# Optimization experiments

Measured on AMD Instinct MI355X. Metric: run time of the kernel, lower is better.

Reference implementation:

```python
import jax, jax.numpy as jnp
import numpy as np

B, S, DIM = 2, 2048, 2048
H, DK, DR, DC, DCP, DV = 16, 128, 64, 512, 1024, 128


def setup_inputs() -> dict:
    key = jax.random.key(0)
    ks = jax.random.split(key, 8)
    s = 0.02  # weight init scale
    return {
        "x": jax.random.normal(ks[0], (B, S, DIM), jnp.float32),
        "W_c": jax.random.normal(ks[1], (DIM, DC), jnp.float32) * s,
        "W_c_prime": jax.random.normal(ks[2], (DIM, DCP), jnp.float32) * s,
        "W_qc": jax.random.normal(ks[3], (H, DCP, DK), jnp.float32) * s,
        "W_qr": jax.random.normal(ks[4], (H, DCP, DR), jnp.float32) * s,
        "W_kc": jax.random.normal(ks[5], (H, DC, DK), jnp.float32) * s,
        "W_kr": jax.random.normal(ks[6], (DIM, DR), jnp.float32) * s,
        "W_v": jax.random.normal(ks[7], (H, DC, DV), jnp.float32) * s,
    }


def reference(x, W_c, W_c_prime, W_qc, W_qr, W_kc, W_kr, W_v):
    # Latent compressions
    c = x @ W_c                 # [B,S,DC]  compressed KV latent
    cp = x @ W_c_prime          # [B,S,DCP] compressed Q latent
    # Per-head projections, vectorized over heads
    q_c = jnp.einsum('bsc,hck->bhsk', cp, W_qc)   # [B,H,S,DK]
    q_r = jnp.einsum('bsc,hcr->bhsr', cp, W_qr)   # [B,H,S,DR]
    k_c = jnp.einsum('bsc,hck->bhsk', c, W_kc)    # [B,H,S,DK]
    k_r = x @ W_kr                                 # [B,S,DR] shared across heads
    q = jnp.concatenate([q_c, q_r], axis=-1)                               # [B,H,S,DK+DR]
    k = jnp.concatenate([k_c, jnp.broadcast_to(k_r[:, None], (B, H, S, DR))], axis=-1)
    scale = 1.0 / np.sqrt(DK + DR)
    scores = jnp.einsum('bhsd,bhtd->bhst', q, k) * scale                   # [B,H,S,S]
    causal = jnp.tril(jnp.ones((S, S), dtype=bool))
    scores = jnp.where(causal, scores, -jnp.inf)
    probs = jax.nn.softmax(scores.astype(jnp.float32), axis=-1).astype(q.dtype)
    v = jnp.einsum('bsc,hcv->bhsv', c, W_v)                                # [B,H,S,DV]
    out = jnp.einsum('bhst,bhtv->bhsv', probs, v)                          # [B,H,S,DV]
    return out.transpose(0, 2, 1, 3).reshape(B, S, H * DV)                 # concat heads
```

## Files before the change

### kernel.cpp

```cpp
#include <hip/hip_runtime.h>
#include <stdint.h>

typedef __bf16 bf16;
typedef __bf16 bfx8 __attribute__((ext_vector_type(8)));
typedef __bf16 bfx4 __attribute__((ext_vector_type(4)));
typedef float floatx4 __attribute__((ext_vector_type(4)));

#define B_ 2
#define S_ 2048
#define DIM_ 2048
#define H_ 16
#define DK_ 128
#define DR_ 64
#define DC_ 512
#define DCP_ 1024
#define DV_ 128
#define DQK_ 192

#define MASK_VAL (-30000.0f)
#define C1_ 0.10411754f

__global__ void k_prep(
    const float* __restrict__ x, bf16* __restrict__ xb,
    const float* __restrict__ W_c, const float* __restrict__ W_cp,
    const float* __restrict__ W_qc, const float* __restrict__ W_qr,
    const float* __restrict__ W_kc, const float* __restrict__ W_kr,
    const float* __restrict__ W_v,
    bf16* __restrict__ Wt_c, bf16* __restrict__ Wt_cp,
    bf16* __restrict__ Wt_qc, bf16* __restrict__ Wt_qr,
    bf16* __restrict__ Wt_kc, bf16* __restrict__ Wt_kr,
    bf16* __restrict__ Wt_v) {
    __shared__ float tile[32][33];
    int bid0 = blockIdx.x;
    if (bid0 < 4096) {
        size_t i = ((size_t)bid0 * 256 + threadIdx.x) * 8;
        float4 a = *(const float4*)(x + i);
        float4 b = *(const float4*)(x + i + 4);
        bfx8 r;
        r[0] = (bf16)a.x; r[1] = (bf16)a.y; r[2] = (bf16)a.z; r[3] = (bf16)a.w;
        r[4] = (bf16)b.x; r[5] = (bf16)b.y; r[6] = (bf16)b.z; r[7] = (bf16)b.w;
        *(bfx8*)(xb + i) = r;
        return;
    }
    int bid = bid0 - 4096;
    const float* in; bf16* out; int K, N, lx, ly, local;
    if (bid < 1024)      { in = W_c;  out = Wt_c;  K = 2048; N = 512;  lx = 4; ly = 6; local = bid; }
    else if (bid < 3072) { in = W_cp; out = Wt_cp; K = 2048; N = 1024; lx = 5; ly = 6; local = bid - 1024; }
    else if (bid < 5120) { in = W_qc; out = Wt_qc; K = 1024; N = 128;  lx = 2; ly = 5; local = bid - 3072; }
    else if (bid < 6144) { in = W_qr; out = Wt_qr; K = 1024; N = 64;   lx = 1; ly = 5; local = bid - 5120; }
    else if (bid < 7168) { in = W_kc; out = Wt_kc; K = 512;  N = 128;  lx = 2; ly = 4; local = bid - 6144; }
    else if (bid < 7296) { in = W_kr; out = Wt_kr; K = 2048; N = 64;   lx = 1; ly = 6; local = bid - 7168; }
    else                 { in = W_v;  out = Wt_v;  K = 512;  N = 128;  lx = 2; ly = 4; local = bid - 7296; }
    int n0 = (local & ((1 << lx) - 1)) << 5;
    int k0 = ((local >> lx) & ((1 << ly) - 1)) << 5;
    int h  = local >> (lx + ly);
    const float* ip = in + (size_t)h * K * N;
    bf16* op = out + (size_t)h * K * N;
    int tx = threadIdx.x & 31, ty = threadIdx.x >> 5;
#pragma unroll
    for (int i = 0; i < 32; i += 8)
        tile[ty + i][tx] = ip[(size_t)(k0 + ty + i) * N + (n0 + tx)];
    __syncthreads();
#pragma unroll
    for (int i = 0; i < 32; i += 8)
        op[(size_t)(n0 + ty + i) * K + (k0 + tx)] = (bf16)tile[tx][ty + i];
}

__device__ __forceinline__ void gld16(const bf16* g, bf16* l) {
    __builtin_amdgcn_global_load_lds(
        (const __attribute__((address_space(1))) void*)g,
        (__attribute__((address_space(3))) void*)l, 16, 0, 0);
}

__device__ __forceinline__ bfx8 frag_ld(const bf16* lds, int row, int quad) {
    int pb = quad ^ ((row >> 1) & 3);
    return *(const bfx8*)(lds + row * 32 + pb * 8);
}

#define SLICE_ 4096

__device__ __forceinline__ void gemm_core(const bf16* __restrict__ A,
                                          const bf16* __restrict__ Bt,
                                          int K, int rowlimB,
                                          floatx4 acc[4][4],
                                          bf16* A_lds, bf16* B_lds) {
    int tid = threadIdx.x, wave = tid >> 6, lane = tid & 63;
    int l15 = lane & 15, quad = lane >> 4;
    int wm = (wave & 1) * 64, wn = (wave >> 1) * 64;
    int ch0 = wave * 2, ch1 = wave * 2 + 1;
    int r0 = ch0 * 16 + (lane >> 2), r1 = ch1 * 16 + (lane >> 2);
    int kb0 = (lane & 3) ^ ((r0 >> 1) & 3), kb1 = (lane & 3) ^ ((r1 >> 1) & 3);
    int rb0 = r0 <= rowlimB ? r0 : rowlimB;
    int rb1 = r1 <= rowlimB ? r1 : rowlimB;
    const bf16* a0 = A + (size_t)r0 * K + kb0 * 8;
    const bf16* a1 = A + (size_t)r1 * K + kb1 * 8;
    const bf16* b0 = Bt + (size_t)rb0 * K + kb0 * 8;
    const bf16* b1 = Bt + (size_t)rb1 * K + kb1 * 8;
    bf16* da0 = A_lds + ch0 * 512;
    bf16* da1 = A_lds + ch1 * 512;
    bf16* db0 = B_lds + ch0 * 512;
    bf16* db1 = B_lds + ch1 * 512;
    for (int k0 = 0; k0 < K; k0 += 64) {
        __syncthreads();
        gld16(a0 + k0, da0);
        gld16(a1 + k0, da1);
        gld16(b0 + k0, db0);
        gld16(b1 + k0, db1);
        gld16(a0 + k0 + 32, da0 + SLICE_);
        gld16(a1 + k0 + 32, da1 + SLICE_);
        gld16(b0 + k0 + 32, db0 + SLICE_);
        gld16(b1 + k0 + 32, db1 + SLICE_);
        __syncthreads();
#pragma unroll
        for (int sl = 0; sl < 2; ++sl) {
            const bf16* As = A_lds + sl * SLICE_;
            const bf16* Bs = B_lds + sl * SLICE_;
            bfx8 a[4], b[4];
#pragma unroll
            for (int t = 0; t < 4; ++t) a[t] = frag_ld(As, wm + t * 16 + l15, quad);
#pragma unroll
            for (int t = 0; t < 4; ++t) b[t] = frag_ld(Bs, wn + t * 16 + l15, quad);
#pragma unroll
            for (int mt = 0; mt < 4; ++mt)
#pragma unroll
                for (int nt = 0; nt < 4; ++nt)
                    acc[mt][nt] = __builtin_amdgcn_mfma_f32_16x16x32_bf16(
                        a[mt], b[nt], acc[mt][nt], 0, 0, 0);
        }
    }
}

__global__ __launch_bounds__(256, 3) void k_gemm1(
    const bf16* __restrict__ xb, const bf16* __restrict__ Wt_c,
    const bf16* __restrict__ Wt_cp, const bf16* __restrict__ Wt_kr,
    bf16* __restrict__ c_ws, bf16* __restrict__ cp_ws, bf16* __restrict__ kr_ws) {
    __shared__ __attribute__((aligned(16))) bf16 A_lds[2 * SLICE_];
    __shared__ __attribute__((aligned(16))) bf16 B_lds[2 * SLICE_];
    int hw = blockIdx.x + 13 * blockIdx.y;
    int virt = (hw & 7) * 52 + (hw >> 3);
    int bx = virt % 13, by = virt / 13;
    const bf16* Bt; bf16* outp; int ldc, col0, rowlim;
    if (bx < 4)       { Bt = Wt_c  + (size_t)bx * 128 * DIM_;       outp = c_ws;  ldc = DC_;  col0 = bx * 128;       rowlim = 127; }
    else if (bx < 12) { Bt = Wt_cp + (size_t)(bx - 4) * 128 * DIM_; outp = cp_ws; ldc = DCP_; col0 = (bx - 4) * 128; rowlim = 127; }
    else              { Bt = Wt_kr;                                  outp = kr_ws; ldc = DR_;  col0 = 0;              rowlim = 63;  }
    floatx4 acc[4][4];
#pragma unroll
    for (int i = 0; i < 4; ++i)
#pragma unroll
        for (int j = 0; j < 4; ++j) acc[i][j] = (floatx4){0.f, 0.f, 0.f, 0.f};
    gemm_core(xb + (size_t)by * 128 * DIM_, Bt, DIM_, rowlim, acc, A_lds, B_lds);
    int tid = threadIdx.x, wave = tid >> 6, lane = tid & 63;
    int l15 = lane & 15, quad = lane >> 4;
    int wm = (wave & 1) * 64, wn = (wave >> 1) * 64;
#pragma unroll
    for (int mt = 0; mt < 4; ++mt)
#pragma unroll
        for (int nt = 0; nt < 4; ++nt) {
            int n = wn + nt * 16 + l15;
            if (n > rowlim) continue;
#pragma unroll
            for (int r = 0; r < 4; ++r) {
                int m = by * 128 + wm + mt * 16 + quad * 4 + r;
                outp[(size_t)m * ldc + col0 + n] = (bf16)acc[mt][nt][r];
            }
        }
}

__global__ __launch_bounds__(256, 3) void k_gemm23(
    const bf16* __restrict__ cp_ws, const bf16* __restrict__ c_ws,
    const bf16* __restrict__ Wt_qc, const bf16* __restrict__ Wt_qr,
    const bf16* __restrict__ Wt_kc, const bf16* __restrict__ Wt_v,
    bf16* __restrict__ q_ws, bf16* __restrict__ kc_ws, bf16* __restrict__ vt_ws) {
    __shared__ __attribute__((aligned(16))) bf16 A_lds[2 * SLICE_];
    __shared__ __attribute__((aligned(16))) bf16 B_lds[2 * SLICE_];
    int hw = blockIdx.x;
    int virt = (hw & 7) * 224 + (hw >> 3);
    int tid = threadIdx.x, wave = tid >> 6, lane = tid & 63;
    int l15 = lane & 15, quad = lane >> 4;
    int wm = (wave & 1) * 64, wn = (wave >> 1) * 64;
    floatx4 acc[4][4];
#pragma unroll
    for (int i = 0; i < 4; ++i)
#pragma unroll
        for (int j = 0; j < 4; ++j) acc[i][j] = (floatx4){0.f, 0.f, 0.f, 0.f};
    if (virt < 768) {
        int bx = virt % 3, by = (virt / 3) & 31, hz = virt / 96;
        const bf16* Bt;
        if (bx < 2) Bt = Wt_qc + (size_t)(hz * 2 + bx) * DK_ * DCP_;
        else        Bt = Wt_qr + (size_t)hz * 128 * DCP_;
        gemm_core(cp_ws + (size_t)by * 128 * DCP_, Bt, DCP_, 127, acc, A_lds, B_lds);
#pragma unroll
        for (int mt = 0; mt < 4; ++mt)
#pragma unroll
            for (int nt = 0; nt < 4; ++nt) {
                int n = wn + nt * 16 + l15;
                int h, col;
                if (bx < 2) { h = hz * 2 + bx;        col = n; }
                else        { h = hz * 2 + (n >> 6);  col = 128 + (n & 63); }
#pragma unroll
                for (int r = 0; r < 4; ++r) {
                    int m = by * 128 + wm + mt * 16 + quad * 4 + r;
                    int b = m >> 11, s = m & 2047;
                    q_ws[(((size_t)b * H_ + h) * S_ + s) * DQK_ + col] =
                        (bf16)(acc[mt][nt][r] * C1_);
                }
            }
    } else {
        int v2 = virt - 768;
        int bx = v2 & 1, by = (v2 >> 1) & 31, h = v2 >> 6;
        const bf16* Bt = (bx == 0) ? (Wt_kc + (size_t)h * DK_ * DC_)
                                   : (Wt_v  + (size_t)h * DV_ * DC_);
        gemm_core(c_ws + (size_t)by * 128 * DC_, Bt, DC_, 127, acc, A_lds, B_lds);
#pragma unroll
        for (int mt = 0; mt < 4; ++mt)
#pragma unroll
            for (int nt = 0; nt < 4; ++nt) {
                int n = wn + nt * 16 + l15;
                if (bx == 0) {
#pragma unroll
                    for (int r = 0; r < 4; ++r) {
                        int m = by * 128 + wm + mt * 16 + quad * 4 + r;
                        int b = m >> 11, s = m & 2047;
                        kc_ws[(((size_t)b * H_ + h) * S_ + s) * DK_ + n] = (bf16)acc[mt][nt][r];
                    }
                } else {
                    int m0 = by * 128 + wm + mt * 16 + quad * 4;
                    int b = m0 >> 11, s = m0 & 2047;
                    bfx4 pack;
#pragma unroll
                    for (int r = 0; r < 4; ++r) pack[r] = (bf16)acc[mt][nt][r];
                    *(bfx4*)(&vt_ws[(((size_t)b * H_ + h) * DV_ + n) * S_ + s]) = pack;
                }
            }
    }
}

__global__ __launch_bounds__(256, 2) void k_attn(
    const bf16* __restrict__ q_ws, const bf16* __restrict__ kc_ws,
    const bf16* __restrict__ kr_ws, const bf16* __restrict__ vt_ws,
    float* __restrict__ out) {
    __shared__ __attribute__((aligned(16))) bf16 K_lds[6 * 2048];
    __shared__ __attribute__((aligned(16))) bf16 V_lds[2 * 4096];
    __shared__ __attribute__((aligned(16))) bf16 P_lds[2 * 2048];
    int hw = blockIdx.x + 16 * blockIdx.y;
    int virt = (hw & 7) * 64 + (hw >> 3);
    int p = virt & 15;
    int bh = virt >> 4, b = bh >> 4, h = bh & 15;
    int tid = threadIdx.x, wave = tid >> 6, lane = tid & 63;
    int l15 = lane & 15, quad = lane >> 4;

    bf16 ov = (bf16)(l15 == 0 ? 1.f : 0.f);
    bfx8 ones8 = {ov, ov, ov, ov, ov, ov, ov, ov};

    int rowk = tid >> 2;
    int kb   = (tid & 3) ^ ((tid >> 3) & 3);
    const bf16* kcp[4]; const bf16* krp[2]; const bf16* vp[4];
#pragma unroll
    for (int j = 0; j < 4; ++j)
        kcp[j] = kc_ws + ((size_t)bh * S_ + rowk) * DK_ + j * 32 + kb * 8;
#pragma unroll
    for (int j = 0; j < 2; ++j)
        krp[j] = kr_ws + ((size_t)b * S_ + rowk) * DR_ + j * 32 + kb * 8;
#pragma unroll
    for (int j = 0; j < 4; ++j)
        vp[j] = vt_ws + ((size_t)bh * DV_ + (j & 1) * 64 + rowk) * S_ + (j >> 1) * 32 + kb * 8;
    bf16* kdst = K_lds + (size_t)tid * 8;
    bf16* vdst = V_lds + (size_t)tid * 8;

    for (int ph = 0; ph < 2; ++ph) {
        int qt = ph ? p : 31 - p;
        int q0 = qt * 64, ntiles = qt + 1;

        const bf16* qrow = q_ws + ((size_t)bh * S_ + q0 + wave * 16 + l15) * DQK_;
        bfx8 qf[6];
#pragma unroll
        for (int ks = 0; ks < 6; ++ks)
            qf[ks] = *(const bfx8*)(qrow + ks * 32 + quad * 8);

        floatx4 o_acc[9];
#pragma unroll
        for (int vt = 0; vt < 9; ++vt) o_acc[vt] = (floatx4){0.f, 0.f, 0.f, 0.f};

        bfx8 pk[4], pr[2], pv[4];
#pragma unroll
        for (int j = 0; j < 4; ++j) pk[j] = *(const bfx8*)(kcp[j]);
#pragma unroll
        for (int j = 0; j < 2; ++j) pr[j] = *(const bfx8*)(krp[j]);
#pragma unroll
        for (int j = 0; j < 4; ++j) pv[j] = *(const bfx8*)(vp[j]);

        for (int t = 0; t < ntiles; ++t) {
            __syncthreads();
#pragma unroll
            for (int j = 0; j < 4; ++j) *(bfx8*)(kdst + j * 2048) = pk[j];
#pragma unroll
            for (int j = 0; j < 2; ++j) *(bfx8*)(kdst + (4 + j) * 2048) = pr[j];
#pragma unroll
            for (int j = 0; j < 4; ++j) *(bfx8*)(vdst + j * 2048) = pv[j];
            __syncthreads();
            if (t + 1 < ntiles) {
                size_t kv1 = (size_t)(t + 1) * 64;
#pragma unroll
                for (int j = 0; j < 4; ++j) pk[j] = *(const bfx8*)(kcp[j] + kv1 * DK_);
#pragma unroll
                for (int j = 0; j < 2; ++j) pr[j] = *(const bfx8*)(krp[j] + kv1 * DR_);
#pragma unroll
                for (int j = 0; j < 4; ++j) pv[j] = *(const bfx8*)(vp[j] + kv1);
            }
            floatx4 sc[4];
#pragma unroll
            for (int nt = 0; nt < 4; ++nt) sc[nt] = (floatx4){0.f, 0.f, 0.f, 0.f};
            __builtin_amdgcn_s_setprio(1);
#pragma unroll
            for (int ks = 0; ks < 6; ++ks)
#pragma unroll
                for (int nt = 0; nt < 4; ++nt) {
                    bfx8 kf = frag_ld(K_lds + ks * 2048, nt * 16 + l15, quad);
                    sc[nt] = __builtin_amdgcn_mfma_f32_16x16x32_bf16(qf[ks], kf, sc[nt], 0, 0, 0);
                }
            __builtin_amdgcn_s_setprio(0);
            if (t == ntiles - 1) {
                int kv0 = t * 64;
#pragma unroll
                for (int nt = 0; nt < 4; ++nt)
#pragma unroll
                    for (int r = 0; r < 4; ++r) {
                        int n_g = kv0 + nt * 16 + l15;
                        int q_g = q0 + wave * 16 + quad * 4 + r;
                        if (n_g > q_g) sc[nt][r] = MASK_VAL;
                    }
            }
#pragma unroll
            for (int nt = 0; nt < 4; ++nt)
#pragma unroll
                for (int r = 0; r < 4; ++r) {
                    int prow = wave * 16 + quad * 4 + r;
                    int pcol = nt * 16 + l15;
                    P_lds[(nt >> 1) * 2048 + prow * 32 +
                          ((((pcol >> 3) & 3) ^ ((prow >> 1) & 3)) * 8) + (pcol & 7)] =
                        (bf16)exp2f(sc[nt][r]);
                }
            __builtin_amdgcn_s_setprio(1);
#pragma unroll
            for (int ks2 = 0; ks2 < 2; ++ks2) {
                bfx8 pf = frag_ld(P_lds + ks2 * 2048, wave * 16 + l15, quad);
#pragma unroll
                for (int vt = 0; vt < 8; ++vt) {
                    bfx8 vf = frag_ld(V_lds + ks2 * 4096, vt * 16 + l15, quad);
                    o_acc[vt] = __builtin_amdgcn_mfma_f32_16x16x32_bf16(pf, vf, o_acc[vt], 0, 0, 0);
                }
                o_acc[8] = __builtin_amdgcn_mfma_f32_16x16x32_bf16(pf, ones8, o_acc[8], 0, 0, 0);
            }
            __builtin_amdgcn_s_setprio(0);
        }
        float rinv[4];
#pragma unroll
        for (int r = 0; r < 4; ++r)
            rinv[r] = 1.f / __shfl(o_acc[8][r], lane & 48);
#pragma unroll
        for (int vt = 0; vt < 8; ++vt)
#pragma unroll
            for (int r = 0; r < 4; ++r) {
                int s = q0 + wave * 16 + quad * 4 + r;
                int v = vt * 16 + l15;
                out[((size_t)b * S_ + s) * (H_ * DV_) + h * DV_ + v] = o_acc[vt][r] * rinv[r];
            }
    }
}

extern "C" void kernel_launch(void* const* d_in, const int* in_sizes, int n_in,
                              void* d_out, int out_size, void* d_ws, size_t ws_size,
                              hipStream_t stream) {
    const float* x    = (const float*)d_in[0];
    const float* W_c  = (const float*)d_in[1];
    const float* W_cp = (const float*)d_in[2];
    const float* W_qc = (const float*)d_in[3];
    const float* W_qr = (const float*)d_in[4];
    const float* W_kc = (const float*)d_in[5];
    const float* W_kr = (const float*)d_in[6];
    const float* W_v  = (const float*)d_in[7];
    float* out = (float*)d_out;

    bf16* c_ws  = (bf16*)d_out;
    bf16* cp_ws = c_ws + (size_t)B_ * S_ * DC_;
    bf16* xb    = cp_ws + (size_t)B_ * S_ * DCP_;

    char* ws = (char*)d_ws;
    size_t off = 0;
    auto alloc = [&](size_t elems) { bf16* p = (bf16*)(ws + off); off += elems * sizeof(bf16); return p; };
    bf16* Wt_c  = alloc((size_t)DIM_ * DC_);
    bf16* Wt_cp = alloc((size_t)DIM_ * DCP_);
    bf16* Wt_qc = alloc((size_t)H_ * DCP_ * DK_);
    bf16* Wt_qr = alloc((size_t)H_ * DCP_ * DR_);
    bf16* Wt_kc = alloc((size_t)H_ * DC_ * DK_);
    bf16* Wt_kr = alloc((size_t)DIM_ * DR_);
    bf16* Wt_v  = alloc((size_t)H_ * DC_ * DV_);
    bf16* kr_ws = alloc((size_t)B_ * S_ * DR_);
    bf16* q_ws  = alloc((size_t)B_ * H_ * S_ * DQK_);
    bf16* kc_ws = alloc((size_t)B_ * H_ * S_ * DK_);
    bf16* vt_ws = alloc((size_t)B_ * H_ * DV_ * S_);

    k_prep<<<dim3(12416), 256, 0, stream>>>(
        x, xb, W_c, W_cp, W_qc, W_qr, W_kc, W_kr, W_v,
        Wt_c, Wt_cp, Wt_qc, Wt_qr, Wt_kc, Wt_kr, Wt_v);

    k_gemm1<<<dim3(13, 32), 256, 0, stream>>>(xb, Wt_c, Wt_cp, Wt_kr, c_ws, cp_ws, kr_ws);
    k_gemm23<<<dim3(1792), 256, 0, stream>>>(cp_ws, c_ws, Wt_qc, Wt_qr, Wt_kc, Wt_v,
                                             q_ws, kc_ws, vt_ws);
    k_attn<<<dim3(16, B_ * H_), 256, 0, stream>>>(q_ws, kc_ws, kr_ws, vt_ws, out);
}
```

Baseline: 294.4 us.

## Retile attention waves into 2x2 row/column grid and regroup gemm23 block mapping

The attention kernel now splits its 64x64 score tile across waves as a 2x2 grid: each wave computes 32 query rows by 32 key columns, then 32 rows by 64 value columns. This halves the redundant K and V fragment loads from LDS per wave, since each fragment is reused across two row tiles. Because waves now read P written by other waves, a __syncthreads is added between the P writes and the PV MMA. Launch bounds drop to 1 block per CU, giving more registers but less occupancy. The gemm23 block-to-work mapping is also changed so blocks sharing XCD index c reuse the same head's weights.

New measurement: 316.9 us. +7.6%, slower.

```diff
diff --git a/kernel.cpp b/kernel.cpp
--- a/kernel.cpp
+++ b/kernel.cpp
@@ -174,7 +174,7 @@
     __shared__ __attribute__((aligned(16))) bf16 A_lds[2 * SLICE_];
     __shared__ __attribute__((aligned(16))) bf16 B_lds[2 * SLICE_];
     int hw = blockIdx.x;
-    int virt = (hw & 7) * 224 + (hw >> 3);
+    int c = hw & 7, idx = hw >> 3;
     int tid = threadIdx.x, wave = tid >> 6, lane = tid & 63;
     int l15 = lane & 15, quad = lane >> 4;
     int wm = (wave & 1) * 64, wn = (wave >> 1) * 64;
@@ -183,8 +183,9 @@
     for (int i = 0; i < 4; ++i)
 #pragma unroll
         for (int j = 0; j < 4; ++j) acc[i][j] = (floatx4){0.f, 0.f, 0.f, 0.f};
-    if (virt < 768) {
-        int bx = virt % 3, by = (virt / 3) & 31, hz = virt / 96;
+    if (idx < 96) {
+        int virt = c * 96 + idx;
+        int bx = virt % 3, by = (virt / 3) & 31, hz = c;
         const bf16* Bt;
         if (bx < 2) Bt = Wt_qc + (size_t)(hz * 2 + bx) * DK_ * DCP_;
         else        Bt = Wt_qr + (size_t)hz * 128 * DCP_;
@@ -206,7 +207,7 @@
                 }
             }
     } else {
-        int v2 = virt - 768;
+        int v2 = c * 128 + (idx - 96);
         int bx = v2 & 1, by = (v2 >> 1) & 31, h = v2 >> 6;
         const bf16* Bt = (bx == 0) ? (Wt_kc + (size_t)h * DK_ * DC_)
                                    : (Wt_v  + (size_t)h * DV_ * DC_);
@@ -235,7 +236,7 @@
     }
 }
 
-__global__ __launch_bounds__(256, 2) void k_attn(
+__global__ __launch_bounds__(256, 1) void k_attn(
     const bf16* __restrict__ q_ws, const bf16* __restrict__ kc_ws,
     const bf16* __restrict__ kr_ws, const bf16* __restrict__ vt_ws,
     float* __restrict__ out) {
@@ -248,6 +249,7 @@
     int bh = virt >> 4, b = bh >> 4, h = bh & 15;
     int tid = threadIdx.x, wave = tid >> 6, lane = tid & 63;
     int l15 = lane & 15, quad = lane >> 4;
+    int rh = wave & 1, ch = wave >> 1;
 
     bf16 ov = (bf16)(l15 == 0 ? 1.f : 0.f);
     bfx8 ones8 = {ov, ov, ov, ov, ov, ov, ov, ov};
@@ -271,15 +273,23 @@
         int qt = ph ? p : 31 - p;
         int q0 = qt * 64, ntiles = qt + 1;
 
-        const bf16* qrow = q_ws + ((size_t)bh * S_ + q0 + wave * 16 + l15) * DQK_;
-        bfx8 qf[6];
-#pragma unroll
-        for (int ks = 0; ks < 6; ++ks)
-            qf[ks] = *(const bfx8*)(qrow + ks * 32 + quad * 8);
-
-        floatx4 o_acc[9];
-#pragma unroll
-        for (int vt = 0; vt < 9; ++vt) o_acc[vt] = (floatx4){0.f, 0.f, 0.f, 0.f};
+        bfx8 qf[2][6];
+#pragma unroll
+        for (int rt = 0; rt < 2; ++rt) {
+            const bf16* qrow =
+                q_ws + ((size_t)bh * S_ + q0 + rh * 32 + rt * 16 + l15) * DQK_;
+#pragma unroll
+            for (int ks = 0; ks < 6; ++ks)
+                qf[rt][ks] = *(const bfx8*)(qrow + ks * 32 + quad * 8);
+        }
+
+        floatx4 o_acc[2][4], l_acc[2];
+#pragma unroll
+        for (int rt = 0; rt < 2; ++rt) {
+            l_acc[rt] = (floatx4){0.f, 0.f, 0.f, 0.f};
+#pragma unroll
+            for (int vt = 0; vt < 4; ++vt) o_acc[rt][vt] = (floatx4){0.f, 0.f, 0.f, 0.f};
+        }
 
         bfx8 pk[4], pr[2], pv[4];
 #pragma unroll
@@ -307,64 +317,79 @@
 #pragma unroll
                 for (int j = 0; j < 4; ++j) pv[j] = *(const bfx8*)(vp[j] + kv1);
             }
-            floatx4 sc[4];
-#pragma unroll
-            for (int nt = 0; nt < 4; ++nt) sc[nt] = (floatx4){0.f, 0.f, 0.f, 0.f};
+            floatx4 sc[2][2];
+#pragma unroll
+            for (int rt = 0; rt < 2; ++rt)
+#pragma unroll
+                for (int ct = 0; ct < 2; ++ct) sc[rt][ct] = (floatx4){0.f, 0.f, 0.f, 0.f};
             __builtin_amdgcn_s_setprio(1);
 #pragma unroll
             for (int ks = 0; ks < 6; ++ks)
 #pragma unroll
-                for (int nt = 0; nt < 4; ++nt) {
-                    bfx8 kf = frag_ld(K_lds + ks * 2048, nt * 16 + l15, quad);
-                    sc[nt] = __builtin_amdgcn_mfma_f32_16x16x32_bf16(qf[ks], kf, sc[nt], 0, 0, 0);
+                for (int ct = 0; ct < 2; ++ct) {
+                    bfx8 kf = frag_ld(K_lds + ks * 2048, ch * 32 + ct * 16 + l15, quad);
+                    sc[0][ct] = __builtin_amdgcn_mfma_f32_16x16x32_bf16(qf[0][ks], kf, sc[0][ct], 0, 0, 0);
+                    sc[1][ct] = __builtin_amdgcn_mfma_f32_16x16x32_bf16(qf[1][ks], kf, sc[1][ct], 0, 0, 0);
                 }
             __builtin_amdgcn_s_setprio(0);
             if (t == ntiles - 1) {
                 int kv0 = t * 64;
 #pragma unroll
-                for (int nt = 0; nt < 4; ++nt)
+                for (int rt = 0; rt < 2; ++rt)
+#pragma unroll
+                    for (int ct = 0; ct < 2; ++ct)
+#pragma unroll
+                        for (int r = 0; r < 4; ++r) {
+                            int n_g = kv0 + ch * 32 + ct * 16 + l15;
+                            int q_g = q0 + rh * 32 + rt * 16 + quad * 4 + r;
+                            if (n_g > q_g) sc[rt][ct][r] = MASK_VAL;
+                        }
+            }
+#pragma unroll
+            for (int rt = 0; rt < 2; ++rt)
+#pragma unroll
+                for (int ct = 0; ct < 2; ++ct)
 #pragma unroll
                     for (int r = 0; r < 4; ++r) {
-                        int n_g = kv0 + nt * 16 + l15;
-                        int q_g = q0 + wave * 16 + quad * 4 + r;
-                        if (n_g > q_g) sc[nt][r] = MASK_VAL;
+                        int prow = rh * 32 + rt * 16 + quad * 4 + r;
+                        int pcol = ch * 32 + ct * 16 + l15;
+                        P_lds[ch * 2048 + prow * 32 +
+                              ((((pcol >> 3) & 3) ^ ((prow >> 1) & 3)) * 8) + (pcol & 7)] =
+                            (bf16)exp2f(sc[rt][ct][r]);
                     }
-            }
-#pragma unroll
-            for (int nt = 0; nt < 4; ++nt)
+            __syncthreads();
+            __builtin_amdgcn_s_setprio(1);
+#pragma unroll
+            for (int ks2 = 0; ks2 < 2; ++ks2) {
+                bfx8 pf0 = frag_ld(P_lds + ks2 * 2048, rh * 32 + l15, quad);
+                bfx8 pf1 = frag_ld(P_lds + ks2 * 2048, rh * 32 + 16 + l15, quad);
+#pragma unroll
+                for (int vt = 0; vt < 4; ++vt) {
+                    bfx8 vf = frag_ld(V_lds + ks2 * 4096, ch * 64 + vt * 16 + l15, quad);
+                    o_acc[0][vt] = __builtin_amdgcn_mfma_f32_16x16x32_bf16(pf0, vf, o_acc[0][vt], 0, 0, 0);
+                    o_acc[1][vt] = __builtin_amdgcn_mfma_f32_16x16x32_bf16(pf1, vf, o_acc[1][vt], 0, 0, 0);
+                }
+                l_acc[0] = __builtin_amdgcn_mfma_f32_16x16x32_bf16(pf0, ones8, l_acc[0], 0, 0, 0);
+                l_acc[1] = __builtin_amdgcn_mfma_f32_16x16x32_bf16(pf1, ones8, l_acc[1], 0, 0, 0);
+            }
+            __builtin_amdgcn_s_setprio(0);
+        }
+#pragma unroll
+        for (int rt = 0; rt < 2; ++rt) {
+            float rinv[4];
+#pragma unroll
+            for (int r = 0; r < 4; ++r)
+                rinv[r] = 1.f / __shfl(l_acc[rt][r], lane & 48);
+#pragma unroll
+            for (int vt = 0; vt < 4; ++vt)
 #pragma unroll
                 for (int r = 0; r < 4; ++r) {
-                    int prow = wave * 16 + quad * 4 + r;
-                    int pcol = nt * 16 + l15;
-                    P_lds[(nt >> 1) * 2048 + prow * 32 +
-                          ((((pcol >> 3) & 3) ^ ((prow >> 1) & 3)) * 8) + (pcol & 7)] =
-                        (bf16)exp2f(sc[nt][r]);
+                    int s = q0 + rh * 32 + rt * 16 + quad * 4 + r;
+                    int v = ch * 64 + vt * 16 + l15;
+                    out[((size_t)b * S_ + s) * (H_ * DV_) + h * DV_ + v] =
+                        o_acc[rt][vt][r] * rinv[r];
                 }
-            __builtin_amdgcn_s_setprio(1);
-#pragma unroll
-            for (int ks2 = 0; ks2 < 2; ++ks2) {
-                bfx8 pf = frag_ld(P_lds + ks2 * 2048, wave * 16 + l15, quad);
-#pragma unroll
-                for (int vt = 0; vt < 8; ++vt) {
-                    bfx8 vf = frag_ld(V_lds + ks2 * 4096, vt * 16 + l15, quad);
-                    o_acc[vt] = __builtin_amdgcn_mfma_f32_16x16x32_bf16(pf, vf, o_acc[vt], 0, 0, 0);
-                }
-                o_acc[8] = __builtin_amdgcn_mfma_f32_16x16x32_bf16(pf, ones8, o_acc[8], 0, 0, 0);
-            }
-            __builtin_amdgcn_s_setprio(0);
-        }
-        float rinv[4];
-#pragma unroll
-        for (int r = 0; r < 4; ++r)
-            rinv[r] = 1.f / __shfl(o_acc[8][r], lane & 48);
-#pragma unroll
-        for (int vt = 0; vt < 8; ++vt)
-#pragma unroll
-            for (int r = 0; r < 4; ++r) {
-                int s = q0 + wave * 16 + quad * 4 + r;
-                int v = vt * 16 + l15;
-                out[((size_t)b * S_ + s) * (H_ * DV_) + h * DV_ + v] = o_acc[vt][r] * rinv[r];
-            }
+        }
     }
 }
 
```
